# Performance work log

Measured on AMD Instinct MI355X. Metric: run time of the kernel, lower is better.

The kernel has to match this reference:

```python
import jax, jax.numpy as jnp
import numpy as np

B, C, N, K, G = 2, 128, 8192, 16, 8
D = C // G
EPS = 1e-5


def _bn(t, g, b, m, v, axis=1):
    # eval-mode BatchNorm: (t - mean) / sqrt(var + eps) * gamma + beta, per channel
    shp = [1] * t.ndim
    shp[axis] = -1
    return (t - m.reshape(shp)) * jax.lax.rsqrt(v.reshape(shp) + EPS) * g.reshape(shp) + b.reshape(shp)


def _knn(xyz, k):
    # brute-force KNN (torch fallback path): xyz (B,3,N) -> idx (B,N,k), includes self
    pts = jnp.transpose(xyz, (0, 2, 1))  # (B,N,3)
    sq = jnp.sum(pts * pts, axis=-1)  # (B,N)
    d2 = sq[:, :, None] + sq[:, None, :] - 2.0 * jnp.einsum('bnc,bmc->bnm', pts, pts)
    _, idx = jax.lax.top_k(-d2, k)  # k smallest squared distances
    return idx


def setup_inputs() -> dict:
    ks = jax.random.split(jax.random.key(0), 16)
    rn = lambda i, s, sc=1.0: jax.random.normal(ks[i], s, jnp.float32) * sc
    sC = C ** -0.5
    return {
        'x': rn(0, (B, C, N)),
        'xyz': rn(1, (B, 3, N)),
        'wq': rn(2, (C, C), sC),
        'bnq_g': jnp.ones((C,)), 'bnq_b': jnp.zeros((C,)), 'bnq_m': jnp.zeros((C,)), 'bnq_v': jnp.ones((C,)),
        'wk': rn(3, (C, C), sC),
        'bnk_g': jnp.ones((C,)), 'bnk_b': jnp.zeros((C,)), 'bnk_m': jnp.zeros((C,)), 'bnk_v': jnp.ones((C,)),
        'wv': rn(4, (C, C), sC),
        'pe_w1': rn(5, (C, 3), 3 ** -0.5),
        'pe_bn_g': jnp.ones((C,)), 'pe_bn_b': jnp.zeros((C,)), 'pe_bn_m': jnp.zeros((C,)), 'pe_bn_v': jnp.ones((C,)),
        'pe_w2': rn(6, (C, C), sC),
        'we_w1': rn(7, (G, C), sC),
        'we_bn_g': jnp.ones((G,)), 'we_bn_b': jnp.zeros((G,)), 'we_bn_m': jnp.zeros((G,)), 'we_bn_v': jnp.ones((G,)),
        'we_w2': rn(8, (G, G), G ** -0.5),
        'wo': rn(9, (C, C), sC),
        'bno_g': jnp.ones((C,)), 'bno_b': jnp.zeros((C,)), 'bno_m': jnp.zeros((C,)), 'bno_v': jnp.ones((C,)),
    }


def reference(x, xyz, wq, bnq_g, bnq_b, bnq_m, bnq_v, wk, bnk_g, bnk_b, bnk_m, bnk_v, wv,
              pe_w1, pe_bn_g, pe_bn_b, pe_bn_m, pe_bn_v, pe_w2,
              we_w1, we_bn_g, we_bn_b, we_bn_m, we_bn_v, we_w2,
              wo, bno_g, bno_b, bno_m, bno_v):
    # q/k/v projections: 1x1 Conv1d == channel matmul
    q = jax.nn.relu(_bn(jnp.einsum('oc,bcn->bon', wq, x), bnq_g, bnq_b, bnq_m, bnq_v))  # (B,C,N)
    kf = jax.nn.relu(_bn(jnp.einsum('oc,bcn->bon', wk, x), bnk_g, bnk_b, bnk_m, bnk_v))
    vf = jnp.einsum('oc,bcn->bon', wv, x)

    idx = _knn(xyz, K)  # (B,N,K)
    bi = jnp.arange(B)[:, None, None]
    kn = jnp.transpose(kf[bi, :, idx], (0, 3, 1, 2))   # (B,C,N,K)
    vn = jnp.transpose(vf[bi, :, idx], (0, 3, 1, 2))   # (B,C,N,K)
    xn = jnp.transpose(xyz[bi, :, idx], (0, 3, 1, 2))  # (B,3,N,K)

    rel = kn - q[:, :, :, None]
    rel_pos = xn - xyz[:, :, :, None]

    # positional encoding MLP (1x1 Conv2d chain)
    pe = jnp.einsum('oc,bcnk->bonk', pe_w2,
                    jax.nn.relu(_bn(jnp.einsum('oc,bcnk->bonk', pe_w1, rel_pos),
                                    pe_bn_g, pe_bn_b, pe_bn_m, pe_bn_v)))
    rel = rel + pe
    vn = vn + pe

    # grouped attention weights over K neighbors
    w = jnp.einsum('hg,bgnk->bhnk', we_w2,
                   jax.nn.relu(_bn(jnp.einsum('gc,bcnk->bgnk', we_w1, rel),
                                   we_bn_g, we_bn_b, we_bn_m, we_bn_v)))  # (B,G,N,K)
    w = jax.nn.softmax(w, axis=-1)

    vg = vn.reshape(B, G, D, N, K)
    out = jnp.einsum('bgdnk,bgnk->bgdn', vg, w).reshape(B, C, N)
    return _bn(jnp.einsum('oc,bcn->bon', wo, out), bno_g, bno_b, bno_m, bno_v)
```

## Files before the change

kernel.cpp:

```cpp
#include <hip/hip_runtime.h>
#include <math.h>

typedef unsigned int u32;
typedef unsigned long long u64;

#define BATCH 2
#define CH 128
#define NPTS 8192
#define KNB 16
#define GRP 8
#define EPSN 1e-5f

#define WS_A     0
#define WS_PW1   4096
#define WS_WE2   6144
#define WS_PTS   8192
#define WS_EQ    270336
#define WS_EK    794624
#define WS_IDX   1318912
#define WS_VFT   2367488

__device__ __forceinline__ float d2f(float4 a, float4 b){
  #pragma clang fp contract(off)
  float dot = a.x*b.x + a.y*b.y + a.z*b.z;
  return (a.w + b.w) - 2.0f*dot;
}
__device__ __forceinline__ u64 shfl_xor_u64(u64 v, int m){
  int lo = __shfl_xor((int)(u32)v, m);
  int hi = __shfl_xor((int)(u32)(v >> 32), m);
  return (((u64)(u32)hi) << 32) | (u32)lo;
}
__device__ __forceinline__ int mbcnt64(u64 bm){
  return (int)__builtin_amdgcn_mbcnt_hi((u32)(bm >> 32),
          __builtin_amdgcn_mbcnt_lo((u32)(bm & 0xFFFFFFFFull), 0u));
}
__device__ __forceinline__ u32 mono32(float d2){
  u32 db = __float_as_uint(d2);
  return (db & 0x80000000u) ? ~db : (db | 0x80000000u);
}

__global__ __launch_bounds__(256) void k0_precomp(
    const float* we_w1, const float* pe_w2, const float* pe_w1,
    const float* we_g, const float* we_v,
    const float* pe_g, const float* pe_b, const float* pe_m, const float* pe_v,
    const float* we_w2, float* wsA, float4* wsPW1, float* wsWE2){
  int t = threadIdx.x;
  for (int i = t; i < 1024; i += 256){
    int g = i >> 7, h = i & 127;
    float s = 0.f;
    for (int c = 0; c < 128; ++c) s = fmaf(we_w1[g*128+c], pe_w2[c*128+h], s);
    float sg = we_g[g] / sqrtf(we_v[g] + EPSN);
    wsA[i] = s * sg;
  }
  if (t < 128){
    float s = pe_g[t] / sqrtf(pe_v[t] + EPSN);
    float bb = pe_b[t] - pe_m[t] * s;
    wsPW1[t] = make_float4(s*pe_w1[t*3+0], s*pe_w1[t*3+1], s*pe_w1[t*3+2], bb);
  }
  if (t < 64) wsWE2[t] = we_w2[t];
}

__global__ __launch_bounds__(256) void k1_pts(const float* xyz, float4* pts){
  int id = blockIdx.x*256 + threadIdx.x;
  if (id >= BATCH*NPTS) return;
  int b = id >> 13, n = id & (NPTS-1);
  float x = xyz[(b*3+0)*NPTS + n];
  float y = xyz[(b*3+1)*NPTS + n];
  float z = xyz[(b*3+2)*NPTS + n];
  float sq;
  {
    #pragma clang fp contract(off)
    sq = (x*x + y*y) + z*z;
  }
  pts[id] = make_float4(x, y, z, sq);
}

#define K2PTS 32
__global__ __launch_bounds__(256) void k2_proj(
    const float* x, const float* wq, const float* wk, const float* wv,
    const float* bnq_g, const float* bnq_b, const float* bnq_m, const float* bnq_v,
    const float* bnk_g, const float* bnk_b, const float* bnk_m, const float* bnk_v,
    const float* we_w1,
    const float* we_g, const float* we_b, const float* we_m, const float* we_v,
    float* eqT, float* ekT, float* vfT){
  __shared__ __align__(16) float qk2[K2PTS][129];
  __shared__ float bnS[128], bnB[128];
  int t = threadIdx.x;
  int mat = blockIdx.x % 3;
  int tmp = blockIdx.x / 3;
  int b   = tmp / (NPTS/K2PTS);
  int n0  = (tmp % (NPTS/K2PTS)) * K2PTS;
  int p = t & 31, og = t >> 5;
  const float* xp = x + (size_t)b*CH*NPTS + n0 + p;
  const float* W = (mat == 0) ? wq : ((mat == 1) ? wk : wv);
  if (mat < 2 && t < 128){
    const float* g_ = mat==0 ? bnq_g : bnk_g;
    const float* b_ = mat==0 ? bnq_b : bnk_b;
    const float* m_ = mat==0 ? bnq_m : bnk_m;
    const float* v_ = mat==0 ? bnq_v : bnk_v;
    float s = g_[t] / sqrtf(v_[t] + EPSN);
    bnS[t] = s;
    bnB[t] = b_[t] - m_[t] * s;
  }
  __syncthreads();
  float acc[16];
  #pragma unroll
  for (int ii = 0; ii < 16; ++ii) acc[ii] = 0.f;
  for (int dd = 0; dd < 32; ++dd){
    float x0 = xp[(size_t)(4*dd+0)*NPTS];
    float x1 = xp[(size_t)(4*dd+1)*NPTS];
    float x2 = xp[(size_t)(4*dd+2)*NPTS];
    float x3 = xp[(size_t)(4*dd+3)*NPTS];
    #pragma unroll
    for (int ii = 0; ii < 16; ++ii){
      int o = og*16 + ii;
      float4 wu = *(const float4*)&W[o*128 + 4*dd];
      acc[ii] = fmaf(wu.x, x0, acc[ii]);
      acc[ii] = fmaf(wu.y, x1, acc[ii]);
      acc[ii] = fmaf(wu.z, x2, acc[ii]);
      acc[ii] = fmaf(wu.w, x3, acc[ii]);
    }
  }
  #pragma unroll
  for (int ii = 0; ii < 16; ++ii){
    int o = og*16 + ii;
    float v = acc[ii];
    if (mat < 2) v = fmaxf(fmaf(bnS[o], v, bnB[o]), 0.f);
    qk2[p][o] = v;
  }
  __syncthreads();
  if (mat < 2){
    int g = t >> 5, pp = t & 31;
    float sg = we_g[g] / sqrtf(we_v[g] + EPSN);
    float tg = we_b[g] - we_m[g] * sg;
    float s = 0.f;
    for (int c4 = 0; c4 < 32; ++c4){
      float4 wv4 = *(const float4*)&we_w1[g*128 + 4*c4];
      float4 qv4 = *(const float4*)&qk2[pp][4*c4];
      s = fmaf(wv4.x, qv4.x, s);
      s = fmaf(wv4.y, qv4.y, s);
      s = fmaf(wv4.z, qv4.z, s);
      s = fmaf(wv4.w, qv4.w, s);
    }
    float val = (mat == 0) ? (tg - sg*s) : (sg*s);
    float* dst = (mat == 0) ? eqT : ekT;
    dst[(b*NPTS + n0 + pp)*8 + g] = val;
  } else {
    #pragma unroll
    for (int i = 0; i < 4; ++i){
      int f = t + 256*i;
      int pp = f >> 5, c4 = (f & 31)*4;
      float4 v = *(const float4*)&qk2[pp][c4];
      *(float4*)&vfT[((size_t)b*NPTS + n0 + pp)*CH + c4] = v;
    }
  }
}

#define QW   2
#define CAPQ 288
__global__ __launch_bounds__(64) void k3_knn(const float4* pts, int* idxout){
  __shared__ u64 smBuf[QW][CAPQ];
  int lane = threadIdx.x;
  int b  = blockIdx.x / (NPTS/QW);
  int q0 = (blockIdx.x % (NPTS/QW)) * QW;
  const float4* P = pts + b*NPTS;

  #pragma unroll
  for (int s = 0; s < QW*CAPQ/64; ++s){
    int f = s*64 + lane;
    smBuf[f / CAPQ][f % CAPQ] = ~0ull;
  }

  float4 qp[QW];
  #pragma unroll
  for (int i = 0; i < QW; ++i) qp[i] = P[q0 + i];

  float T[QW];
  {
    float v0 = 3.402823466e38f, v1 = 3.402823466e38f;
    #pragma unroll
    for (int j = 0; j < 16; ++j){
      float4 c = P[lane + 64*j];
      v0 = fminf(v0, d2f(qp[0], c));
      v1 = fminf(v1, d2f(qp[1], c));
    }
    float t0 = v0, t1 = v1;
    #pragma unroll
    for (int r = 0; r < 16; ++r){
      float m0 = v0, m1 = v1;
      #pragma unroll
      for (int msk = 1; msk <= 32; msk <<= 1){
        m0 = fminf(m0, __shfl_xor(m0, msk));
        m1 = fminf(m1, __shfl_xor(m1, msk));
      }
      if (v0 == m0) v0 = 3.402823466e38f;
      if (v1 == m1) v1 = 3.402823466e38f;
      t0 = m0; t1 = m1;
    }
    T[0] = t0; T[1] = t1;
  }

  float Tlo[QW], Thi[QW]; int cnt[QW];
  #pragma unroll
  for (int i = 0; i < QW; ++i){ Tlo[i] = -3.0e38f; Thi[i] = 3.0e38f; cnt[i] = 0; }
  auto step = [&](float4 c, u32 m, int i){
    float d2 = d2f(qp[i], c);
    bool pred = d2 <= T[i];
    u64 bm = __ballot(pred);
    if (bm){
      int cc = __popcll(bm);
      if (pred && cnt[i] + cc <= CAPQ){
        int pos = cnt[i] + mbcnt64(bm);
        smBuf[i][pos] = (((u64)mono32(d2)) << 32) | m;
      }
      cnt[i] += cc;
    }
  };
  bool anybad = true;
  for (int att = 0; att < 16 && anybad; ++att){
    #pragma unroll
    for (int i = 0; i < QW; ++i) cnt[i] = 0;
    float4 c0 = P[lane], c1 = P[64 + lane], c2 = P[128 + lane], c3 = P[192 + lane];
    for (int base = 0; base < NPTS; base += 256){
      float4 e0 = c0, e1 = c1, e2 = c2, e3 = c3;
      int nb = base + 256;
      if (nb < NPTS){
        c0 = P[nb       + lane];
        c1 = P[nb +  64 + lane];
        c2 = P[nb + 128 + lane];
        c3 = P[nb + 192 + lane];
      }
      #pragma unroll
      for (int i = 0; i < QW; ++i){
        step(e0, (u32)(base       + lane), i);
        step(e1, (u32)(base +  64 + lane), i);
        step(e2, (u32)(base + 128 + lane), i);
        step(e3, (u32)(base + 192 + lane), i);
      }
    }
    anybad = false;
    #pragma unroll
    for (int i = 0; i < QW; ++i){
      if (cnt[i] > CAPQ){
        Thi[i] = T[i];
        T[i] = (Tlo[i] > -3.0e38f) ? 0.5f*(Tlo[i] + Thi[i])
                                   : ((T[i] > 0.f) ? T[i]*0.5f : T[i]*2.0f - 1.0f);
        anybad = true;
      } else if (cnt[i] < 16){
        Tlo[i] = T[i];
        T[i] = 0.5f*(Tlo[i] + Thi[i]);
        anybad = true;
      }
    }
  }

  {
    int cq0 = cnt[0] < CAPQ ? cnt[0] : CAPQ;
    int cq1 = cnt[1] < CAPQ ? cnt[1] : CAPQ;
    u64 a0, a1, a2, a3, a4, b0, b1, b2, b3, b4;
    a0 = (lane       < cq0) ? smBuf[0][lane      ] : ~0ull;
    a1 = (lane +  64 < cq0) ? smBuf[0][lane +  64] : ~0ull;
    a2 = (lane + 128 < cq0) ? smBuf[0][lane + 128] : ~0ull;
    a3 = (lane + 192 < cq0) ? smBuf[0][lane + 192] : ~0ull;
    a4 = (lane + 256 < cq0) ? smBuf[0][lane + 256] : ~0ull;
    b0 = (lane       < cq1) ? smBuf[1][lane      ] : ~0ull;
    b1 = (lane +  64 < cq1) ? smBuf[1][lane +  64] : ~0ull;
    b2 = (lane + 128 < cq1) ? smBuf[1][lane + 128] : ~0ull;
    b3 = (lane + 192 < cq1) ? smBuf[1][lane + 192] : ~0ull;
    b4 = (lane + 256 < cq1) ? smBuf[1][lane + 256] : ~0ull;
    #define CE_(x,y) { if (y < x){ u64 tm_ = x; x = y; y = tm_; } }
    CE_(a0,a1) CE_(a1,a2) CE_(a2,a3) CE_(a3,a4)
    CE_(a0,a1) CE_(a1,a2) CE_(a2,a3)
    CE_(a0,a1) CE_(a1,a2)
    CE_(a0,a1)
    CE_(b0,b1) CE_(b1,b2) CE_(b2,b3) CE_(b3,b4)
    CE_(b0,b1) CE_(b1,b2) CE_(b2,b3)
    CE_(b0,b1) CE_(b1,b2)
    CE_(b0,b1)
    #undef CE_
    int nq0 = q0, nq1 = q0 + 1;
    #pragma unroll
    for (int r = 0; r < 16; ++r){
      u64 g0 = a0, g1 = b0;
      #pragma unroll
      for (int msk = 1; msk <= 32; msk <<= 1){
        u64 o0 = shfl_xor_u64(g0, msk);
        u64 o1 = shfl_xor_u64(g1, msk);
        g0 = (o0 < g0) ? o0 : g0;
        g1 = (o1 < g1) ? o1 : g1;
      }
      if (a0 == g0){ a0 = a1; a1 = a2; a2 = a3; a3 = a4; a4 = ~0ull; }
      if (b0 == g1){ b0 = b1; b1 = b2; b2 = b3; b3 = b4; b4 = ~0ull; }
      if (lane == 0){
        idxout[(b*NPTS + nq0)*16 + r] = (g0 == ~0ull) ? nq0 : (int)(g0 & (u32)(NPTS-1));
        idxout[(b*NPTS + nq1)*16 + r] = (g1 == ~0ull) ? nq1 : (int)(g1 & (u32)(NPTS-1));
      }
    }
  }
}

#define H2S 136
__global__ __launch_bounds__(256, 4) void k4_attn(
    const float4* pts, const float* eqT, const float* ekT, const int* idxw,
    const float* vfT, const float* wsA, const float4* wsPW1, const float* wsWE2,
    const float* pe_w2, const float* wo,
    const float* bno_g, const float* bno_b, const float* bno_m, const float* bno_v,
    float* out){
  __shared__ __align__(16) float4 smW1[128];
  __shared__ __align__(16) float4 smP[4][16];
  __shared__ int   smJ[4][16];
  __shared__ float smw[4][16][8];
  __shared__ __align__(16) float smH[4][8][H2S];
  __shared__ __align__(16) float smOutv[4][128];
  int t = threadIdx.x;
  int wv = t >> 6, lane = t & 63;
  int b  = blockIdx.x >> 11;
  int n0 = (blockIdx.x & 2047) * 4;
  if (t < 128) smW1[t] = wsPW1[t];
  __syncthreads();

  int n = n0 + wv;
  int gq = b*NPTS + n;
  int k = lane >> 2, q = lane & 3;

  {
    float4 pn  = pts[gq];
    float4 eqa = *(const float4*)&eqT[gq*8];
    float4 eqb = *(const float4*)&eqT[gq*8+4];
    int j = idxw[gq*16 + k] & (NPTS-1);
    int gj = b*NPTS + j;
    float4 pj  = pts[gj];
    float4 eka = *(const float4*)&ekT[gj*8];
    float4 ekb = *(const float4*)&ekT[gj*8+4];
    float rx = pj.x - pn.x, ry = pj.y - pn.y, rz = pj.z - pn.z;
    if (q == 0){
      smP[wv][k] = make_float4(rx, ry, rz, 0.f);
      smJ[wv][k] = j;
    }
    float ee[8] = {eka.x+eqa.x, eka.y+eqa.y, eka.z+eqa.z, eka.w+eqa.w,
                   ekb.x+eqb.x, ekb.y+eqb.y, ekb.z+eqb.z, ekb.w+eqb.w};
    float lp[8] = {0.f,0.f,0.f,0.f,0.f,0.f,0.f,0.f};
    #pragma unroll
    for (int i = 0; i < 8; ++i){
      int hb = 4*q + 16*i;
      float4 w1;
      w1 = smW1[hb+0]; float hv0 = fmaxf(fmaf(w1.x, rx, fmaf(w1.y, ry, fmaf(w1.z, rz, w1.w))), 0.f);
      w1 = smW1[hb+1]; float hv1 = fmaxf(fmaf(w1.x, rx, fmaf(w1.y, ry, fmaf(w1.z, rz, w1.w))), 0.f);
      w1 = smW1[hb+2]; float hv2 = fmaxf(fmaf(w1.x, rx, fmaf(w1.y, ry, fmaf(w1.z, rz, w1.w))), 0.f);
      w1 = smW1[hb+3]; float hv3 = fmaxf(fmaf(w1.x, rx, fmaf(w1.y, ry, fmaf(w1.z, rz, w1.w))), 0.f);
      #pragma unroll
      for (int g = 0; g < 8; ++g){
        float4 a4 = *(const float4*)&wsA[g*128 + hb];
        lp[g] = fmaf(a4.x, hv0, lp[g]);
        lp[g] = fmaf(a4.y, hv1, lp[g]);
        lp[g] = fmaf(a4.z, hv2, lp[g]);
        lp[g] = fmaf(a4.w, hv3, lp[g]);
      }
    }
    #pragma unroll
    for (int g = 0; g < 8; ++g){
      lp[g] += __shfl_xor(lp[g], 1);
      lp[g] += __shfl_xor(lp[g], 2);
      lp[g] = fmaxf(lp[g] + ee[g], 0.f);
    }
    float lo0 = 0.f, lo1 = 0.f;
    #pragma unroll
    for (int g = 0; g < 8; ++g){
      lo0 = fmaf(wsWE2[(2*q+0)*8 + g], lp[g], lo0);
      lo1 = fmaf(wsWE2[(2*q+1)*8 + g], lp[g], lo1);
    }
    float m0 = lo0, m1 = lo1;
    #pragma unroll
    for (int msk = 4; msk <= 32; msk <<= 1){
      m0 = fmaxf(m0, __shfl_xor(m0, msk));
      m1 = fmaxf(m1, __shfl_xor(m1, msk));
    }
    float e0 = __expf(lo0 - m0), e1 = __expf(lo1 - m1);
    float s0 = e0, s1 = e1;
    #pragma unroll
    for (int msk = 4; msk <= 32; msk <<= 1){
      s0 += __shfl_xor(s0, msk);
      s1 += __shfl_xor(s1, msk);
    }
    smw[wv][k][2*q+0] = e0 / s0;
    smw[wv][k][2*q+1] = e1 / s1;
  }

  {
    int g3 = lane >> 3, hh = lane & 7;
    float4 H4[4];
    #pragma unroll
    for (int ii = 0; ii < 4; ++ii) H4[ii] = make_float4(0.f,0.f,0.f,0.f);
    for (int kk = 0; kk < 16; ++kk){
      float4 r4 = smP[wv][kk];
      float wg  = smw[wv][kk][g3];
      #pragma unroll
      for (int ii = 0; ii < 4; ++ii){
        int hb = 4*hh + 32*ii;
        float4 w1;
        w1 = smW1[hb+0]; float hv0 = fmaxf(fmaf(w1.x, r4.x, fmaf(w1.y, r4.y, fmaf(w1.z, r4.z, w1.w))), 0.f);
        w1 = smW1[hb+1]; float hv1 = fmaxf(fmaf(w1.x, r4.x, fmaf(w1.y, r4.y, fmaf(w1.z, r4.z, w1.w))), 0.f);
        w1 = smW1[hb+2]; float hv2 = fmaxf(fmaf(w1.x, r4.x, fmaf(w1.y, r4.y, fmaf(w1.z, r4.z, w1.w))), 0.f);
        w1 = smW1[hb+3]; float hv3 = fmaxf(fmaf(w1.x, r4.x, fmaf(w1.y, r4.y, fmaf(w1.z, r4.z, w1.w))), 0.f);
        H4[ii].x = fmaf(wg, hv0, H4[ii].x);
        H4[ii].y = fmaf(wg, hv1, H4[ii].y);
        H4[ii].z = fmaf(wg, hv2, H4[ii].z);
        H4[ii].w = fmaf(wg, hv3, H4[ii].w);
      }
    }
    #pragma unroll
    for (int ii = 0; ii < 4; ++ii)
      *(float4*)&smH[wv][g3][4*hh + 32*ii] = H4[ii];
  }
  __syncthreads();

  if (t < 128){
    int c = t, g = c >> 4;
    float acc[4] = {0.f, 0.f, 0.f, 0.f};
    for (int i = 0; i < 32; ++i){
      float4 pw = *(const float4*)&pe_w2[c*128 + 4*i];
      #pragma unroll
      for (int pt = 0; pt < 4; ++pt){
        float4 h4 = *(const float4*)&smH[pt][g][4*i];
        acc[pt] = fmaf(pw.x, h4.x, acc[pt]);
        acc[pt] = fmaf(pw.y, h4.y, acc[pt]);
        acc[pt] = fmaf(pw.z, h4.z, acc[pt]);
        acc[pt] = fmaf(pw.w, h4.w, acc[pt]);
      }
    }
    #pragma unroll
    for (int pt = 0; pt < 4; ++pt){
      #pragma unroll
      for (int kk = 0; kk < 16; ++kk){
        int jj = smJ[pt][kk];
        float wgk = smw[pt][kk][g];
        acc[pt] = fmaf(wgk, vfT[((size_t)b*NPTS + jj)*CH + c], acc[pt]);
      }
      smOutv[pt][c] = acc[pt];
    }
  }
  __syncthreads();

  if (t < 128){
    int o = t;
    float so = bno_g[o] / sqrtf(bno_v[o] + EPSN);
    float bo = bno_b[o] - bno_m[o] * so;
    float fa[4] = {0.f, 0.f, 0.f, 0.f};
    for (int i = 0; i < 32; ++i){
      float4 pw = *(const float4*)&wo[o*128 + 4*i];
      #pragma unroll
      for (int pt = 0; pt < 4; ++pt){
        float4 h4 = *(const float4*)&smOutv[pt][4*i];
        fa[pt] = fmaf(pw.x, h4.x, fa[pt]);
        fa[pt] = fmaf(pw.y, h4.y, fa[pt]);
        fa[pt] = fmaf(pw.z, h4.z, fa[pt]);
        fa[pt] = fmaf(pw.w, h4.w, fa[pt]);
      }
    }
    float4 st;
    st.x = fmaf(so, fa[0], bo);
    st.y = fmaf(so, fa[1], bo);
    st.z = fmaf(so, fa[2], bo);
    st.w = fmaf(so, fa[3], bo);
    *(float4*)&out[((size_t)b*CH + o)*NPTS + n0] = st;
  }
}

extern "C" void kernel_launch(void* const* d_in, const int* in_sizes, int n_in,
                              void* d_out, int out_size, void* d_ws, size_t ws_size,
                              hipStream_t stream){
  const float* x     = (const float*)d_in[0];
  const float* xyz   = (const float*)d_in[1];
  const float* wq    = (const float*)d_in[2];
  const float* bnq_g = (const float*)d_in[3];
  const float* bnq_b = (const float*)d_in[4];
  const float* bnq_m = (const float*)d_in[5];
  const float* bnq_v = (const float*)d_in[6];
  const float* wk    = (const float*)d_in[7];
  const float* bnk_g = (const float*)d_in[8];
  const float* bnk_b = (const float*)d_in[9];
  const float* bnk_m = (const float*)d_in[10];
  const float* bnk_v = (const float*)d_in[11];
  const float* wv    = (const float*)d_in[12];
  const float* pe_w1 = (const float*)d_in[13];
  const float* pe_g  = (const float*)d_in[14];
  const float* pe_b  = (const float*)d_in[15];
  const float* pe_m  = (const float*)d_in[16];
  const float* pe_v  = (const float*)d_in[17];
  const float* pe_w2 = (const float*)d_in[18];
  const float* we_w1 = (const float*)d_in[19];
  const float* we_g  = (const float*)d_in[20];
  const float* we_b  = (const float*)d_in[21];
  const float* we_m  = (const float*)d_in[22];
  const float* we_v  = (const float*)d_in[23];
  const float* we_w2 = (const float*)d_in[24];
  const float* wo    = (const float*)d_in[25];
  const float* bno_g = (const float*)d_in[26];
  const float* bno_b = (const float*)d_in[27];
  const float* bno_m = (const float*)d_in[28];
  const float* bno_v = (const float*)d_in[29];

  char* ws = (char*)d_ws;
  float*  wsA   = (float*)(ws + WS_A);
  float4* wsPW1 = (float4*)(ws + WS_PW1);
  float*  wsWE2 = (float*)(ws + WS_WE2);
  float4* pts   = (float4*)(ws + WS_PTS);
  float*  eqT   = (float*)(ws + WS_EQ);
  float*  ekT   = (float*)(ws + WS_EK);
  int*    idxw  = (int*)(ws + WS_IDX);
  float*  vfT   = (float*)(ws + WS_VFT);
  float*  outp  = (float*)d_out;

  k0_precomp<<<dim3(1), dim3(256), 0, stream>>>(we_w1, pe_w2, pe_w1, we_g, we_v,
                                                pe_g, pe_b, pe_m, pe_v, we_w2,
                                                wsA, wsPW1, wsWE2);
  k1_pts<<<dim3(64), dim3(256), 0, stream>>>(xyz, pts);
  k2_proj<<<dim3(BATCH*(NPTS/K2PTS)*3), dim3(256), 0, stream>>>(x, wq, wk, wv,
                                               bnq_g, bnq_b, bnq_m, bnq_v,
                                               bnk_g, bnk_b, bnk_m, bnk_v,
                                               we_w1, we_g, we_b, we_m, we_v,
                                               eqT, ekT, vfT);
  k3_knn<<<dim3(BATCH*(NPTS/QW)), dim3(64), 0, stream>>>(pts, idxw);
  k4_attn<<<dim3(BATCH*(NPTS/4)), dim3(256), 0, stream>>>(pts, eqT, ekT, idxw, vfT,
                                                wsA, wsPW1, wsWE2, pe_w2, wo,
                                                bno_g, bno_b, bno_m, bno_v, outp);
}
```

Baseline: 351.2 us.

## Fuse projection and KNN kernels into one heterogeneous launch

Merges the q/k/v projection kernel and the brute-force KNN kernel into a single launch. Blocks are interleaved in groups of 7: three do the projection work and four each pack four 64-thread KNN waves. The two independent stages can then run concurrently, which fills the GPU better and removes one launch boundary. In exchange, all blocks share one dynamic LDS size and 256-thread launch bounds, which may lower KNN occupancy, and any intra-KNN synchronisation must still be correct at wave granularity.

```diff
diff --git a/kernel.cpp b/kernel.cpp
--- a/kernel.cpp
+++ b/kernel.cpp
@@ -76,93 +76,102 @@
 }
 
 #define K2PTS 32
-__global__ __launch_bounds__(256) void k2_proj(
+#define QW   2
+#define CAPQ 288
+#define K23_LDS 18432
+__global__ __launch_bounds__(256) void k23_fused(
     const float* x, const float* wq, const float* wk, const float* wv,
     const float* bnq_g, const float* bnq_b, const float* bnq_m, const float* bnq_v,
     const float* bnk_g, const float* bnk_b, const float* bnk_m, const float* bnk_v,
     const float* we_w1,
     const float* we_g, const float* we_b, const float* we_m, const float* we_v,
-    float* eqT, float* ekT, float* vfT){
-  __shared__ __align__(16) float qk2[K2PTS][129];
-  __shared__ float bnS[128], bnB[128];
+    float* eqT, float* ekT, float* vfT,
+    const float4* pts, int* idxout){
+  extern __shared__ __align__(16) char smRaw[];
   int t = threadIdx.x;
-  int mat = blockIdx.x % 3;
-  int tmp = blockIdx.x / 3;
-  int b   = tmp / (NPTS/K2PTS);
-  int n0  = (tmp % (NPTS/K2PTS)) * K2PTS;
-  int p = t & 31, og = t >> 5;
-  const float* xp = x + (size_t)b*CH*NPTS + n0 + p;
-  const float* W = (mat == 0) ? wq : ((mat == 1) ? wk : wv);
-  if (mat < 2 && t < 128){
-    const float* g_ = mat==0 ? bnq_g : bnk_g;
-    const float* b_ = mat==0 ? bnq_b : bnk_b;
-    const float* m_ = mat==0 ? bnq_m : bnk_m;
-    const float* v_ = mat==0 ? bnq_v : bnk_v;
-    float s = g_[t] / sqrtf(v_[t] + EPSN);
-    bnS[t] = s;
-    bnB[t] = b_[t] - m_[t] * s;
-  }
-  __syncthreads();
-  float acc[16];
-  #pragma unroll
-  for (int ii = 0; ii < 16; ++ii) acc[ii] = 0.f;
-  for (int dd = 0; dd < 32; ++dd){
-    float x0 = xp[(size_t)(4*dd+0)*NPTS];
-    float x1 = xp[(size_t)(4*dd+1)*NPTS];
-    float x2 = xp[(size_t)(4*dd+2)*NPTS];
-    float x3 = xp[(size_t)(4*dd+3)*NPTS];
+  int grp = blockIdx.x / 7, rem = blockIdx.x % 7;
+
+  if (rem < 3){
+    float (*qk2)[129] = (float(*)[129])smRaw;
+    float* bnS = (float*)(smRaw + 16512);
+    float* bnB = (float*)(smRaw + 17024);
+    int bid2 = grp*3 + rem;
+    int mat = bid2 % 3;
+    int tmp = bid2 / 3;
+    int b   = tmp / (NPTS/K2PTS);
+    int n0  = (tmp % (NPTS/K2PTS)) * K2PTS;
+    int p = t & 31, og = t >> 5;
+    const float* xp = x + (size_t)b*CH*NPTS + n0 + p;
+    const float* W = (mat == 0) ? wq : ((mat == 1) ? wk : wv);
+    if (mat < 2 && t < 128){
+      const float* g_ = mat==0 ? bnq_g : bnk_g;
+      const float* b_ = mat==0 ? bnq_b : bnk_b;
+      const float* m_ = mat==0 ? bnq_m : bnk_m;
+      const float* v_ = mat==0 ? bnq_v : bnk_v;
+      float s = g_[t] / sqrtf(v_[t] + EPSN);
+      bnS[t] = s;
+      bnB[t] = b_[t] - m_[t] * s;
+    }
+    __syncthreads();
+    float acc[16];
+    #pragma unroll
+    for (int ii = 0; ii < 16; ++ii) acc[ii] = 0.f;
+    for (int dd = 0; dd < 32; ++dd){
+      float x0 = xp[(size_t)(4*dd+0)*NPTS];
+      float x1 = xp[(size_t)(4*dd+1)*NPTS];
+      float x2 = xp[(size_t)(4*dd+2)*NPTS];
+      float x3 = xp[(size_t)(4*dd+3)*NPTS];
+      #pragma unroll
+      for (int ii = 0; ii < 16; ++ii){
+        int o = og*16 + ii;
+        float4 wu = *(const float4*)&W[o*128 + 4*dd];
+        acc[ii] = fmaf(wu.x, x0, acc[ii]);
+        acc[ii] = fmaf(wu.y, x1, acc[ii]);
+        acc[ii] = fmaf(wu.z, x2, acc[ii]);
+        acc[ii] = fmaf(wu.w, x3, acc[ii]);
+      }
+    }
     #pragma unroll
     for (int ii = 0; ii < 16; ++ii){
       int o = og*16 + ii;
-      float4 wu = *(const float4*)&W[o*128 + 4*dd];
-      acc[ii] = fmaf(wu.x, x0, acc[ii]);
-      acc[ii] = fmaf(wu.y, x1, acc[ii]);
-      acc[ii] = fmaf(wu.z, x2, acc[ii]);
-      acc[ii] = fmaf(wu.w, x3, acc[ii]);
-    }
-  }
-  #pragma unroll
-  for (int ii = 0; ii < 16; ++ii){
-    int o = og*16 + ii;
-    float v = acc[ii];
-    if (mat < 2) v = fmaxf(fmaf(bnS[o], v, bnB[o]), 0.f);
-    qk2[p][o] = v;
-  }
-  __syncthreads();
-  if (mat < 2){
-    int g = t >> 5, pp = t & 31;
-    float sg = we_g[g] / sqrtf(we_v[g] + EPSN);
-    float tg = we_b[g] - we_m[g] * sg;
-    float s = 0.f;
-    for (int c4 = 0; c4 < 32; ++c4){
-      float4 wv4 = *(const float4*)&we_w1[g*128 + 4*c4];
-      float4 qv4 = *(const float4*)&qk2[pp][4*c4];
-      s = fmaf(wv4.x, qv4.x, s);
-      s = fmaf(wv4.y, qv4.y, s);
-      s = fmaf(wv4.z, qv4.z, s);
-      s = fmaf(wv4.w, qv4.w, s);
-    }
-    float val = (mat == 0) ? (tg - sg*s) : (sg*s);
-    float* dst = (mat == 0) ? eqT : ekT;
-    dst[(b*NPTS + n0 + pp)*8 + g] = val;
-  } else {
-    #pragma unroll
-    for (int i = 0; i < 4; ++i){
-      int f = t + 256*i;
-      int pp = f >> 5, c4 = (f & 31)*4;
-      float4 v = *(const float4*)&qk2[pp][c4];
-      *(float4*)&vfT[((size_t)b*NPTS + n0 + pp)*CH + c4] = v;
-    }
-  }
-}
-
-#define QW   2
-#define CAPQ 288
-__global__ __launch_bounds__(64) void k3_knn(const float4* pts, int* idxout){
-  __shared__ u64 smBuf[QW][CAPQ];
-  int lane = threadIdx.x;
-  int b  = blockIdx.x / (NPTS/QW);
-  int q0 = (blockIdx.x % (NPTS/QW)) * QW;
+      float v = acc[ii];
+      if (mat < 2) v = fmaxf(fmaf(bnS[o], v, bnB[o]), 0.f);
+      qk2[p][o] = v;
+    }
+    __syncthreads();
+    if (mat < 2){
+      int g = t >> 5, pp = t & 31;
+      float sg = we_g[g] / sqrtf(we_v[g] + EPSN);
+      float tg = we_b[g] - we_m[g] * sg;
+      float s = 0.f;
+      for (int c4 = 0; c4 < 32; ++c4){
+        float4 wv4 = *(const float4*)&we_w1[g*128 + 4*c4];
+        float4 qv4 = *(const float4*)&qk2[pp][4*c4];
+        s = fmaf(wv4.x, qv4.x, s);
+        s = fmaf(wv4.y, qv4.y, s);
+        s = fmaf(wv4.z, qv4.z, s);
+        s = fmaf(wv4.w, qv4.w, s);
+      }
+      float val = (mat == 0) ? (tg - sg*s) : (sg*s);
+      float* dst = (mat == 0) ? eqT : ekT;
+      dst[(b*NPTS + n0 + pp)*8 + g] = val;
+    } else {
+      #pragma unroll
+      for (int i = 0; i < 4; ++i){
+        int f = t + 256*i;
+        int pp = f >> 5, c4 = (f & 31)*4;
+        float4 v = *(const float4*)&qk2[pp][c4];
+        *(float4*)&vfT[((size_t)b*NPTS + n0 + pp)*CH + c4] = v;
+      }
+    }
+    return;
+  }
+
+  int wv3 = t >> 6, lane = t & 63;
+  u64 (*smBuf)[CAPQ] = (u64(*)[CAPQ])(smRaw + wv3*(QW*CAPQ*8));
+  int unit = (grp*4 + (rem - 3))*4 + wv3;
+  int b  = unit / (NPTS/QW);
+  int q0 = (unit % (NPTS/QW)) * QW;
   const float4* P = pts + b*NPTS;
 
   #pragma unroll
@@ -515,12 +524,11 @@
                                                 pe_g, pe_b, pe_m, pe_v, we_w2,
                                                 wsA, wsPW1, wsWE2);
   k1_pts<<<dim3(64), dim3(256), 0, stream>>>(xyz, pts);
-  k2_proj<<<dim3(BATCH*(NPTS/K2PTS)*3), dim3(256), 0, stream>>>(x, wq, wk, wv,
+  k23_fused<<<dim3(3584), dim3(256), K23_LDS, stream>>>(x, wq, wk, wv,
                                                bnq_g, bnq_b, bnq_m, bnq_v,
                                                bnk_g, bnk_b, bnk_m, bnk_v,
                                                we_w1, we_g, we_b, we_m, we_v,
-                                               eqT, ekT, vfT);
-  k3_knn<<<dim3(BATCH*(NPTS/QW)), dim3(64), 0, stream>>>(pts, idxw);
+                                               eqT, ekT, vfT, pts, idxw);
   k4_attn<<<dim3(BATCH*(NPTS/4)), dim3(256), 0, stream>>>(pts, eqT, ekT, idxw, vfT,
                                                 wsA, wsPW1, wsWE2, pe_w2, wo,
                                                 bno_g, bno_b, bno_m, bno_v, outp);
```

Result: faster. 327.7 us (-6.7%).
